# Kernel tuning notes

Hardware: AMD Instinct MI355X
Metric: run time of the kernel (lower is better)

The kernel has to match this reference:

```python
import jax, jax.numpy as jnp
import numpy as np

RADIUS = 12
SIGMA = 5.0
T0 = 0.1
TOP_PERCENT = 0.1
CURVE_STEPS = 8


def _gaussian_kernel():
    xs = jnp.arange(-RADIUS, RADIUS + 1, dtype=jnp.float32)
    k = jnp.exp(-0.5 * jnp.square(xs / SIGMA))
    k = k / jnp.sum(k)
    k2 = k[:, None] * k[None, :]
    # depthwise kernel (O=3, I/group=1, 25, 25)
    return jnp.tile(k2[None, None], (3, 1, 1, 1))


def tanh01(x):
    return (jnp.tanh(x) + 1) / 2


def tanh_range(l, r):
    return lambda x: tanh01(x) * (r - l) + l


def _parse_params(p):
    omega = tanh_range(0.1, 1.0)(p[:, 0:1])                          # (B,1)
    wb_mask = jnp.array([0.0, 1.0, 1.0], dtype=p.dtype)[None]
    wb = jnp.exp(tanh_range(-0.5, 0.5)(p[:, 1:4] * wb_mask))         # (B,3)
    lg = jnp.log(jnp.asarray(3.0, dtype=p.dtype))
    gamma = jnp.exp(tanh_range(-lg, lg)(p[:, 4:5]))                  # (B,1)
    tone = tanh_range(0.5, 2.0)(p[:, 5:13].reshape(-1, 1, 8)[:, None, None, :])  # (B,1,1,1,8)
    contrast = jnp.tanh(p[:, 13:14])                                 # (B,1)
    sharpen = tanh_range(0.0, 5.0)(p[:, 14:15])                      # (B,1)
    return omega, wb, gamma, tone, contrast, sharpen


def _apply_defog(x, omega):
    # mirror `if x.min() < 0: x = (x+1)/2` in a jit-safe way
    x = jnp.where(jnp.min(x) < 0, (x + 1) / 2, x)
    B, C, H, W = x.shape
    dark = jnp.min(x, axis=1)                                        # (B,H,W)
    k = int(H * W * TOP_PERCENT)
    flat = dark.reshape(B, H * W)
    _, idx = jax.lax.top_k(flat, k)                                  # (B,k)
    xf = x.reshape(B, C, H * W)
    sel = jnp.take_along_axis(xf, idx[:, None, :], axis=2)           # (B,C,k)
    A = jnp.max(sel, axis=2)[:, :, None, None]                       # (B,C,1,1)
    t = jnp.clip(1 - omega[:, :, None] * dark, T0, 1.0)[:, None]     # (B,1,H,W)
    J = (x - A) / t + A
    return jnp.clip(J, 0.0, 1.0)


def _apply_white_balance(image, wb):
    denom = (0.27 * wb[:, 0] + 0.67 * wb[:, 1] + 0.06 * wb[:, 2] + 1e-05)[:, None]
    p = wb / denom
    return image * p[:, :, None, None]


def _apply_gamma(image, gamma):
    g = jnp.tile(gamma, (1, 3))[:, :, None, None]                    # (B,3,1,1)
    return jnp.power(jnp.maximum(image, 1e-4), g)


def _apply_tone(image, tone):
    tone_sum = jnp.sum(tone, axis=-1) + 1e-30                        # (B,1,1,1)
    total = jnp.zeros_like(image)
    for i in range(CURVE_STEPS):
        total = total + jnp.clip(image - 1.0 * i / CURVE_STEPS, 0.0, 1.0 / CURVE_STEPS) * tone[:, :, :, :, i]
    return total * CURVE_STEPS / tone_sum


def _apply_contrast(image, contrast):
    # faithful to source: rgb2lum indexes the LAST axis (W), giving (B,3,H,1)
    lum = (0.27 * image[:, :, :, 0] + 0.67 * image[:, :, :, 1] + 0.06 * image[:, :, :, 2])[:, :, :, None]
    lum = jnp.clip(lum, 0.0, 1.0)
    contrast_lum = -jnp.cos(jnp.pi * lum) * 0.5 + 0.5
    contrast_image = image / (lum + 1e-6) * contrast_lum
    c = contrast[:, :, None, None]                                   # (B,1,1,1)
    return (1 - c) * image + c * contrast_image


def _apply_sharpen(image, sharpen):
    kernel = _gaussian_kernel()
    blurred = jax.lax.conv_general_dilated(
        image, kernel, window_strides=(1, 1),
        padding=[(RADIUS, RADIUS), (RADIUS, RADIUS)],
        dimension_numbers=('NCHW', 'OIHW', 'NCHW'),
        feature_group_count=3)
    s = sharpen[:, None, None, :]                                    # (B,1,1,1)
    return (image - blurred) * s + image


def setup_inputs() -> dict:
    key = jax.random.key(0)
    k1, k2 = jax.random.split(key)
    x = jax.random.uniform(k1, (16, 3, 512, 512), dtype=jnp.float32)
    params = jax.random.normal(k2, (16, 15), dtype=jnp.float32)
    return {"x": x, "params": params}


def reference(x, params):
    omega, wb, gamma, tone, contrast, sharpen = _parse_params(params)
    image = _apply_defog(x, omega)
    image = _apply_white_balance(image, wb)
    image = _apply_gamma(image, gamma)
    image = _apply_tone(image, tone)
    image = _apply_contrast(image, contrast)
    image = _apply_sharpen(image, sharpen)
    return jax.nn.sigmoid(image)
```

## Files before the change

kernel.cpp:

```cpp
#include <hip/hip_runtime.h>
#include <math.h>

#define NB 16
#define NC 3
#define NH 512
#define NW 512
#define NHW (NH*NW)
#define KSEL 26214u
#define PI_F 3.14159265358979f
#define LOG2E_F 1.44269504f
#define POISON_U32 0xAAAAAAAAu

typedef _Float16 half4v __attribute__((ext_vector_type(4)));
typedef _Float16 half8v __attribute__((ext_vector_type(8)));
typedef float    float4v __attribute__((ext_vector_type(4)));

#define TMPH_OFF   0
#define PCH_OFF    (NB*NC*NHW/2)
#define HIST_OFF   (PCH_OFF + NB*NC*NHW/2)
#define BMAX_OFF   (HIST_OFF + NB*256)
#define AVAL_OFF   (BMAX_OFF + NB*768)
#define PBUF_OFF   (AVAL_OFF + NB*3)
#define GW_OFF     (PBUF_OFF + NB*32)

__device__ __forceinline__ float fast_rcp(float x)  { return __builtin_amdgcn_rcpf(x); }
__device__ __forceinline__ float fast_exp2(float x) { return __builtin_amdgcn_exp2f(x); }
__device__ __forceinline__ float fast_log2(float x) { return __builtin_amdgcn_logf(x); }

__device__ __forceinline__ int swzf4(int f) {
  int t = f & 7;
  int g = ((f >> 3) & 1) ? ((3 - t) & 7) : t;
  return (f & ~7) | g;
}

__device__ __forceinline__ float chain_tt(float xv, float dv, float omega, float Aval,
                                          float wbp, float g, const float* tone) {
  float t = fminf(fmaxf(1.f - omega*dv, 0.1f), 1.f);
  float J = (xv - Aval)*fast_rcp(t) + Aval;
  J = fminf(fmaxf(J, 0.f), 1.f);
  float v = J * wbp;
  float u = fast_exp2(g * fast_log2(fmaxf(v, 1e-4f)));
  float tt = 0.f;
#pragma unroll
  for (int i = 0; i < 8; i++)
    tt = fmaf(fminf(fmaxf(u - 0.125f*(float)i, 0.f), 0.125f), tone[i], tt);
  return tt;
}

__device__ __forceinline__ float4 chain4(float4 v, float4 d, float omega, float A,
                                         float wbp, float g, const float* tone) {
  float4 r;
  r.x = chain_tt(v.x, d.x, omega, A, wbp, g, tone);
  r.y = chain_tt(v.y, d.y, omega, A, wbp, g, tone);
  r.z = chain_tt(v.z, d.z, omega, A, wbp, g, tone);
  r.w = chain_tt(v.w, d.w, omega, A, wbp, g, tone);
  return r;
}

__global__ __launch_bounds__(256) void k_stats(const float* __restrict__ x,
                                               unsigned* __restrict__ hist,
                                               unsigned* __restrict__ binmax) {
  __shared__ unsigned lh[8*256];
  __shared__ unsigned lbm[8][768];
  int tid = threadIdx.x, b = blockIdx.y;
  for (int i = tid; i < 8*256; i += 256) lh[i] = 0u;
  for (int i = tid; i < 8*768; i += 256) ((unsigned*)lbm)[i] = 0u;
  __syncthreads();
  const float4* x0 = (const float4*)(x + (size_t)b*NC*NHW);
  const float4* x1 = x0 + NHW/4;
  const float4* x2 = x1 + NHW/4;
  unsigned* lhm = lh + (tid & 7)*256;
  unsigned* bmr = lbm[tid & 7];
  int base = blockIdx.x*1024 + tid;
#pragma unroll
  for (int it = 0; it < 4; it++) {
    int i = base + it*256;
    float4 a = x0[i], g = x1[i], r = x2[i];
    float dv[4] = { fminf(fminf(a.x,g.x),r.x), fminf(fminf(a.y,g.y),r.y),
                    fminf(fminf(a.z,g.z),r.z), fminf(fminf(a.w,g.w),r.w) };
    float av[4] = {a.x,a.y,a.z,a.w}, gv[4] = {g.x,g.y,g.z,g.w}, rv[4] = {r.x,r.y,r.z,r.w};
#pragma unroll
    for (int q = 0; q < 4; q++) {
      unsigned bin = __float_as_uint(dv[q]) >> 24;
      atomicAdd(&lhm[bin], 1u);
      atomicMax(&bmr[bin],       __float_as_uint(av[q]));
      atomicMax(&bmr[256 + bin], __float_as_uint(gv[q]));
      atomicMax(&bmr[512 + bin], __float_as_uint(rv[q]));
    }
  }
  __syncthreads();
  {
    unsigned s = 0;
    for (int r2 = 0; r2 < 8; r2++) s += lh[r2*256 + tid];
    if (s) atomicAdd(&hist[b*256 + tid], s);
  }
  for (int idx = tid; idx < 768; idx += 256) {
    unsigned m = lbm[0][idx];
#pragma unroll
    for (int r2 = 1; r2 < 8; r2++) m = max(m, lbm[r2][idx]);
    if (m) atomicMin(&binmax[b*768 + idx], 0x7FFFFFFFu - m);
  }
}

__global__ void k_scan(const unsigned* __restrict__ hist,
                       const unsigned* __restrict__ binmax,
                       float* __restrict__ avals,
                       const float* __restrict__ p, float* __restrict__ pbuf,
                       float* __restrict__ gw) {
  int b = blockIdx.x, tid = threadIdx.x;
  if (tid < 64) {
    int lane = tid;
    unsigned cnt[4], s = 0;
#pragma unroll
    for (int j = 0; j < 4; j++) {
      cnt[j] = hist[b*256 + (255 - (lane*4+j))] - POISON_U32;
      s += cnt[j];
    }
    unsigned inc = s;
    for (int off = 1; off < 64; off <<= 1) {
      unsigned n = __shfl_up(inc, off);
      if (lane >= off) inc += n;
    }
    unsigned excl = inc - s;
    bool found = (excl < KSEL && KSEL <= inc);
    int localBin = 0;
    if (found) {
      unsigned run = excl; int binj = 0;
#pragma unroll
      for (int j = 0; j < 4; j++) {
        unsigned nb = run + cnt[j];
        if (KSEL > run && KSEL <= nb) binj = j;
        run = nb;
      }
      localBin = 255 - (lane*4 + binj);
    }
    unsigned long long mask = __ballot(found ? 1 : 0);
    int src = (int)__ffsll((long long)mask) - 1;
    int bstar = __shfl(localBin, src);
#pragma unroll
    for (int c = 0; c < 3; c++) {
      float m = 0.f;
#pragma unroll
      for (int j = 0; j < 4; j++) {
        int bin = 255 - (lane*4 + j);
        if (bin >= bstar) {
          unsigned enc = binmax[b*768 + c*256 + bin];
          unsigned bits = (enc <= 0x7FFFFFFFu) ? (0x7FFFFFFFu - enc) : 0u;
          m = fmaxf(m, __uint_as_float(bits));
        }
      }
      for (int off = 1; off < 64; off <<= 1) m = fmaxf(m, __shfl_xor(m, off));
      if (lane == 0) avals[b*3 + c] = m;
    }
  } else if (tid == 64) {
    const float* pp = p + b*15;
    float* ob = pbuf + b*32;
    float omega = (tanhf(pp[0])+1.f)*0.5f*0.9f + 0.1f;
    float wb0 = 1.0f;
    float wb1 = expf((tanhf(pp[2])+1.f)*0.5f - 0.5f);
    float wb2 = expf((tanhf(pp[3])+1.f)*0.5f - 0.5f);
    float denom = 0.27f*wb0 + 0.67f*wb1 + 0.06f*wb2 + 1e-5f;
    float lg = logf(3.0f);
    float g = expf((tanhf(pp[4])+1.f)*0.5f*(2.f*lg) - lg);
    float ts = 0.f, tone[8];
    for (int i = 0; i < 8; i++) { tone[i] = (tanhf(pp[5+i])+1.f)*0.5f*1.5f + 0.5f; ts += tone[i]; }
    ts += 1e-30f;
    ob[0] = omega; ob[1] = wb0/denom; ob[2] = wb1/denom; ob[3] = wb2/denom; ob[4] = g;
    for (int i = 0; i < 8; i++) ob[5+i] = tone[i];
    ob[13] = 8.0f/ts;
    ob[14] = tanhf(pp[13]);
    ob[15] = (tanhf(pp[14])+1.f)*0.5f*5.0f;
  } else if (tid == 65 && b == 0) {
    float wv[25], wsum = 0.f;
    for (int i = 0; i < 25; i++) { float d = (float)(i-12)/5.0f; wv[i] = expf(-0.5f*d*d); wsum += wv[i]; }
    for (int i = 0; i < 25; i++) gw[i] = wv[i]/wsum;
  }
}

__global__ __launch_bounds__(256) void k_hblur(
    const float* __restrict__ x, const float* __restrict__ pbuf,
    const float* __restrict__ avals, const float* __restrict__ gw,
    _Float16* __restrict__ tmph, _Float16* __restrict__ pch) {
  __shared__ __align__(16) float pcp[4][544];
  int tid = threadIdx.x;
  int row = tid >> 6, lane = tid & 63;
  int b = blockIdx.y, c = blockIdx.z;
  int h = blockIdx.x*4 + row;
  const float* pb = pbuf + b*32;
  float omega = pb[0], g = pb[4], ts = pb[13], cc = pb[14];
  float wbp = pb[1 + c];
  float tone[8];
#pragma unroll
  for (int i = 0; i < 8; i++) tone[i] = pb[5+i];
  float A = avals[b*3 + c];
  if (lane < 4) {
    float4 z; z.x = 0.f; z.y = 0.f; z.z = 0.f; z.w = 0.f;
    *(float4*)(&pcp[row][0] + swzf4(lane)*4) = z;
    *(float4*)(&pcp[row][0] + swzf4(132 + lane)*4) = z;
  }
  const float* xbase = x + (size_t)b*3*NHW + (size_t)h*NW;
  const float4* xr0 = (const float4*)(xbase);
  const float4* xr1 = (const float4*)(xbase + NHW);
  const float4* xr2 = (const float4*)(xbase + 2*(size_t)NHW);
  float4 pk;
#pragma unroll
  for (int m = 0; m < 2; m++) {
    int i4 = lane + m*64;
    float4 v0 = xr0[i4], v1 = xr1[i4], v2 = xr2[i4];
    float4 d;
    d.x = fminf(fminf(v0.x,v1.x),v2.x); d.y = fminf(fminf(v0.y,v1.y),v2.y);
    d.z = fminf(fminf(v0.z,v1.z),v2.z); d.w = fminf(fminf(v0.w,v1.w),v2.w);
    float4 vc = (c == 0) ? v0 : (c == 1) ? v1 : v2;
    float4 p = chain4(vc, d, omega, A, wbp, g, tone);
    *(float4*)(&pcp[row][0] + swzf4(4 + i4)*4) = p;
    if (m == 0) pk = p;
  }
  __syncthreads();
  float rf;
  {
    float t0 = 0.f;
    if (lane == 0) {
      float l = fminf(fmaxf((0.27f*pk.x + 0.67f*pk.y + 0.06f*pk.z)*ts, 0.f), 1.f);
      t0 = ts*((1.f - cc) + cc*(0.5f - 0.5f*__cosf(PI_F*l))*fast_rcp(l + 1e-6f));
    }
    rf = __shfl(t0, 0);
  }
  float kw[25];
#pragma unroll
  for (int j = 0; j < 25; j++) kw[j] = gw[j];
  float4 w[8];
#pragma unroll
  for (int r = 0; r < 8; r++) w[r] = *(const float4*)(&pcp[row][0] + swzf4(2*lane + 1 + r)*4);
  float acc[8] = {0,0,0,0,0,0,0,0};
#pragma unroll
  for (int r = 0; r < 8; r++) {
    float vs[4] = {w[r].x, w[r].y, w[r].z, w[r].w};
#pragma unroll
    for (int q = 0; q < 4; q++) {
      int idx = r*4 + q;
#pragma unroll
      for (int i = 0; i < 8; i++) {
        int j = idx - i;
        if (j >= 0 && j < 25) acc[i] = fmaf(kw[j], vs[q], acc[i]);
      }
    }
  }
  size_t off = ((size_t)b*3 + c)*NHW + (size_t)h*NW + lane*8;
  half8v th;
#pragma unroll
  for (int i = 0; i < 8; i++) th[i] = (_Float16)(acc[i]*rf);
  *(half8v*)(tmph + off) = th;
  half8v ph;
  ph[0] = (_Float16)(w[3].x*rf); ph[1] = (_Float16)(w[3].y*rf);
  ph[2] = (_Float16)(w[3].z*rf); ph[3] = (_Float16)(w[3].w*rf);
  ph[4] = (_Float16)(w[4].x*rf); ph[5] = (_Float16)(w[4].y*rf);
  ph[6] = (_Float16)(w[4].z*rf); ph[7] = (_Float16)(w[4].w*rf);
  *(half8v*)(pch + off) = ph;
}

#define VSTR 68
__global__ __launch_bounds__(256) void k_vblur(
    const _Float16* __restrict__ tmph, const _Float16* __restrict__ pch,
    const float* __restrict__ pbuf, const float* __restrict__ gw,
    float* __restrict__ out) {
  __shared__ _Float16 sh[152*VSTR];
  int tid = threadIdx.x;
  int bc = blockIdx.z, b = bc/3;
  int w0 = blockIdx.x*64, h0 = blockIdx.y*128;
  const _Float16* tr = tmph + (size_t)bc*NHW;
  for (int idx = tid; idx < 152*8; idx += 256) {
    int r = idx >> 3, seg = idx & 7;
    int gh = h0 - 12 + r;
    uint4 v = make_uint4(0u,0u,0u,0u);
    if (gh >= 0 && gh < NH) v = *(const uint4*)(tr + (size_t)gh*NW + w0 + seg*8);
    _Float16* dst = &sh[r*VSTR + seg*8];
    uint2 lo; lo.x = v.x; lo.y = v.y;
    uint2 hi; hi.x = v.z; hi.y = v.w;
    *(uint2*)dst = lo;
    *(uint2*)(dst + 4) = hi;
  }
  __syncthreads();
  float kw[25];
#pragma unroll
  for (int j = 0; j < 25; j++) kw[j] = gw[j];
  int wq = tid & 15, rg = tid >> 4;
  int rowbase = rg*8;
  float4v acc[8];
#pragma unroll
  for (int i = 0; i < 8; i++) acc[i] = (float4v)0.f;
#pragma unroll
  for (int r = 0; r < 32; r++) {
    half4v hv = *(const half4v*)&sh[(rowbase + r)*VSTR + wq*4];
    float4v v = __builtin_convertvector(hv, float4v);
#pragma unroll
    for (int i = 0; i < 8; i++) {
      int j = r - i;
      if (j >= 0 && j < 25) acc[i] += kw[j]*v;
    }
  }
  float sharp = pbuf[b*32 + 15];
#pragma unroll
  for (int i = 0; i < 8; i++) {
    int h = h0 + rowbase + i;
    size_t off = (size_t)bc*NHW + (size_t)h*NW + w0 + wq*4;
    half4v pcv = *(const half4v*)(pch + off);
    float4v pc = __builtin_convertvector(pcv, float4v);
    float4v res = (pc - acc[i])*sharp + pc;
    float4v o;
    o.x = fast_rcp(1.f + fast_exp2(-res.x*LOG2E_F));
    o.y = fast_rcp(1.f + fast_exp2(-res.y*LOG2E_F));
    o.z = fast_rcp(1.f + fast_exp2(-res.z*LOG2E_F));
    o.w = fast_rcp(1.f + fast_exp2(-res.w*LOG2E_F));
    *(float4v*)(out + off) = o;
  }
}

extern "C" void kernel_launch(void* const* d_in, const int* in_sizes, int n_in,
                              void* d_out, int out_size, void* d_ws, size_t ws_size,
                              hipStream_t stream) {
  const float* x = (const float*)d_in[0];
  const float* params = (const float*)d_in[1];
  float* out = (float*)d_out;
  float* ws = (float*)d_ws;

  _Float16* tmph = (_Float16*)(ws + TMPH_OFF);
  _Float16* pch  = (_Float16*)(ws + PCH_OFF);
  unsigned* hist   = (unsigned*)(ws + HIST_OFF);
  unsigned* binmax = (unsigned*)(ws + BMAX_OFF);
  float* avals = ws + AVAL_OFF;
  float* pbuf  = ws + PBUF_OFF;
  float* gw    = ws + GW_OFF;

  k_stats<<<dim3(64, NB), 256, 0, stream>>>(x, hist, binmax);
  k_scan<<<NB, 128, 0, stream>>>(hist, binmax, avals, params, pbuf, gw);
  k_hblur<<<dim3(NH/4, NB, 3), 256, 0, stream>>>(x, pbuf, avals, gw, tmph, pch);
  k_vblur<<<dim3(NW/64, NH/128, NB*NC), 256, 0, stream>>>(tmph, pch, pbuf, gw, out);
}
```

Baseline: 152.9 us.

## Process all three channels per hblur block and use wave shuffles for halo

The horizontal blur kernel now handles all three channels of a row in one block. It computes the dark-channel min once, so x is read once instead of three times across separate channel blocks. The shared-memory row buffer and __syncthreads are replaced with cross-lane shuffles that fetch neighbour pixels for the 25-tap horizontal convolution. The trade-off is more shuffle instructions and more registers per thread, and only a third as many blocks are launched.

```diff
diff --git a/kernel.cpp b/kernel.cpp
--- a/kernel.cpp
+++ b/kernel.cpp
@@ -27,12 +27,6 @@
 __device__ __forceinline__ float fast_exp2(float x) { return __builtin_amdgcn_exp2f(x); }
 __device__ __forceinline__ float fast_log2(float x) { return __builtin_amdgcn_logf(x); }
 
-__device__ __forceinline__ int swzf4(int f) {
-  int t = f & 7;
-  int g = ((f >> 3) & 1) ? ((3 - t) & 7) : t;
-  return (f & ~7) | g;
-}
-
 __device__ __forceinline__ float chain_tt(float xv, float dv, float omega, float Aval,
                                           float wbp, float g, const float* tone) {
   float t = fminf(fmaxf(1.f - omega*dv, 0.1f), 1.f);
@@ -45,16 +39,6 @@
   for (int i = 0; i < 8; i++)
     tt = fmaf(fminf(fmaxf(u - 0.125f*(float)i, 0.f), 0.125f), tone[i], tt);
   return tt;
-}
-
-__device__ __forceinline__ float4 chain4(float4 v, float4 d, float omega, float A,
-                                         float wbp, float g, const float* tone) {
-  float4 r;
-  r.x = chain_tt(v.x, d.x, omega, A, wbp, g, tone);
-  r.y = chain_tt(v.y, d.y, omega, A, wbp, g, tone);
-  r.z = chain_tt(v.z, d.z, omega, A, wbp, g, tone);
-  r.w = chain_tt(v.w, d.w, omega, A, wbp, g, tone);
-  return r;
 }
 
 __global__ __launch_bounds__(256) void k_stats(const float* __restrict__ x,
@@ -181,81 +165,111 @@
     const float* __restrict__ x, const float* __restrict__ pbuf,
     const float* __restrict__ avals, const float* __restrict__ gw,
     _Float16* __restrict__ tmph, _Float16* __restrict__ pch) {
-  __shared__ __align__(16) float pcp[4][544];
   int tid = threadIdx.x;
-  int row = tid >> 6, lane = tid & 63;
-  int b = blockIdx.y, c = blockIdx.z;
-  int h = blockIdx.x*4 + row;
+  int wv = tid >> 6, lane = tid & 63;
+  int b = blockIdx.y;
+  int h = blockIdx.x*4 + wv;
   const float* pb = pbuf + b*32;
   float omega = pb[0], g = pb[4], ts = pb[13], cc = pb[14];
-  float wbp = pb[1 + c];
+  float wbp[3] = {pb[1], pb[2], pb[3]};
   float tone[8];
 #pragma unroll
   for (int i = 0; i < 8; i++) tone[i] = pb[5+i];
-  float A = avals[b*3 + c];
-  if (lane < 4) {
-    float4 z; z.x = 0.f; z.y = 0.f; z.z = 0.f; z.w = 0.f;
-    *(float4*)(&pcp[row][0] + swzf4(lane)*4) = z;
-    *(float4*)(&pcp[row][0] + swzf4(132 + lane)*4) = z;
-  }
+  float Av[3] = {avals[b*3], avals[b*3+1], avals[b*3+2]};
+  float kw[25];
+#pragma unroll
+  for (int j = 0; j < 25; j++) kw[j] = gw[j];
+
   const float* xbase = x + (size_t)b*3*NHW + (size_t)h*NW;
-  const float4* xr0 = (const float4*)(xbase);
-  const float4* xr1 = (const float4*)(xbase + NHW);
-  const float4* xr2 = (const float4*)(xbase + 2*(size_t)NHW);
-  float4 pk;
-#pragma unroll
-  for (int m = 0; m < 2; m++) {
-    int i4 = lane + m*64;
-    float4 v0 = xr0[i4], v1 = xr1[i4], v2 = xr2[i4];
-    float4 d;
-    d.x = fminf(fminf(v0.x,v1.x),v2.x); d.y = fminf(fminf(v0.y,v1.y),v2.y);
-    d.z = fminf(fminf(v0.z,v1.z),v2.z); d.w = fminf(fminf(v0.w,v1.w),v2.w);
-    float4 vc = (c == 0) ? v0 : (c == 1) ? v1 : v2;
-    float4 p = chain4(vc, d, omega, A, wbp, g, tone);
-    *(float4*)(&pcp[row][0] + swzf4(4 + i4)*4) = p;
-    if (m == 0) pk = p;
-  }
-  __syncthreads();
-  float rf;
+  float cv[8], d[8];
   {
-    float t0 = 0.f;
-    if (lane == 0) {
-      float l = fminf(fmaxf((0.27f*pk.x + 0.67f*pk.y + 0.06f*pk.z)*ts, 0.f), 1.f);
-      t0 = ts*((1.f - cc) + cc*(0.5f - 0.5f*__cosf(PI_F*l))*fast_rcp(l + 1e-6f));
-    }
-    rf = __shfl(t0, 0);
-  }
-  float kw[25];
-#pragma unroll
-  for (int j = 0; j < 25; j++) kw[j] = gw[j];
-  float4 w[8];
-#pragma unroll
-  for (int r = 0; r < 8; r++) w[r] = *(const float4*)(&pcp[row][0] + swzf4(2*lane + 1 + r)*4);
-  float acc[8] = {0,0,0,0,0,0,0,0};
-#pragma unroll
-  for (int r = 0; r < 8; r++) {
-    float vs[4] = {w[r].x, w[r].y, w[r].z, w[r].w};
+    const float4* r0 = (const float4*)xbase;
+    const float4* r1 = (const float4*)(xbase + NHW);
+    const float4* r2 = (const float4*)(xbase + 2*(size_t)NHW);
+    float4 a0 = r0[2*lane], a1 = r0[2*lane+1];
+    float4 b0 = r1[2*lane], b1 = r1[2*lane+1];
+    float4 c0 = r2[2*lane], c1 = r2[2*lane+1];
+    d[0] = fminf(fminf(a0.x,b0.x),c0.x); d[1] = fminf(fminf(a0.y,b0.y),c0.y);
+    d[2] = fminf(fminf(a0.z,b0.z),c0.z); d[3] = fminf(fminf(a0.w,b0.w),c0.w);
+    d[4] = fminf(fminf(a1.x,b1.x),c1.x); d[5] = fminf(fminf(a1.y,b1.y),c1.y);
+    d[6] = fminf(fminf(a1.z,b1.z),c1.z); d[7] = fminf(fminf(a1.w,b1.w),c1.w);
+    cv[0]=a0.x; cv[1]=a0.y; cv[2]=a0.z; cv[3]=a0.w;
+    cv[4]=a1.x; cv[5]=a1.y; cv[6]=a1.z; cv[7]=a1.w;
+  }
+  bool okm1 = (lane >= 1), okm2 = (lane >= 2);
+  bool okp1 = (lane <= 62), okp2 = (lane <= 61);
+
+#pragma unroll
+  for (int c = 0; c < 3; c++) {
+    if (c > 0) {
+      const float4* xr = (const float4*)(xbase + (size_t)c*NHW);
+      asm volatile("" : "+v"(xr));
+      float4 u0 = xr[2*lane], u1 = xr[2*lane+1];
+      cv[0]=u0.x; cv[1]=u0.y; cv[2]=u0.z; cv[3]=u0.w;
+      cv[4]=u1.x; cv[5]=u1.y; cv[6]=u1.z; cv[7]=u1.w;
+    }
+    float pv[8];
+#pragma unroll
+    for (int k = 0; k < 8; k++) pv[k] = chain_tt(cv[k], d[k], omega, Av[c], wbp[c], g, tone);
+    float l0 = __shfl(pv[0], 0), l1 = __shfl(pv[1], 0), l2 = __shfl(pv[2], 0);
+    float l = fminf(fmaxf((0.27f*l0 + 0.67f*l1 + 0.06f*l2)*ts, 0.f), 1.f);
+    float rf = ts*((1.f - cc) + cc*(0.5f - 0.5f*__cosf(PI_F*l))*fast_rcp(l + 1e-6f));
+    float acc[8] = {0,0,0,0,0,0,0,0};
+#pragma unroll
+    for (int q = 0; q < 8; q++)
+#pragma unroll
+      for (int j = 0; j < 8; j++)
+        acc[j] = fmaf(kw[q-j+12], pv[q], acc[j]);
+#pragma unroll
+    for (int q = 0; q < 8; q++) {
+      float v = __shfl(pv[q], lane-1);
+      v = okm1 ? v : 0.f;
+#pragma unroll
+      for (int j = 0; j < 8; j++) {
+        int t = -8 + q - j;
+        if (t >= -12) acc[j] = fmaf(kw[t+12], v, acc[j]);
+      }
+    }
+#pragma unroll
+    for (int q = 0; q < 8; q++) {
+      float v = __shfl(pv[q], lane+1);
+      v = okp1 ? v : 0.f;
+#pragma unroll
+      for (int j = 0; j < 8; j++) {
+        int t = 8 + q - j;
+        if (t <= 12) acc[j] = fmaf(kw[t+12], v, acc[j]);
+      }
+    }
+#pragma unroll
+    for (int q = 4; q < 8; q++) {
+      float v = __shfl(pv[q], lane-2);
+      v = okm2 ? v : 0.f;
+#pragma unroll
+      for (int j = 0; j < 8; j++) {
+        int t = -16 + q - j;
+        if (t >= -12) acc[j] = fmaf(kw[t+12], v, acc[j]);
+      }
+    }
 #pragma unroll
     for (int q = 0; q < 4; q++) {
-      int idx = r*4 + q;
-#pragma unroll
-      for (int i = 0; i < 8; i++) {
-        int j = idx - i;
-        if (j >= 0 && j < 25) acc[i] = fmaf(kw[j], vs[q], acc[i]);
-      }
-    }
-  }
-  size_t off = ((size_t)b*3 + c)*NHW + (size_t)h*NW + lane*8;
-  half8v th;
-#pragma unroll
-  for (int i = 0; i < 8; i++) th[i] = (_Float16)(acc[i]*rf);
-  *(half8v*)(tmph + off) = th;
-  half8v ph;
-  ph[0] = (_Float16)(w[3].x*rf); ph[1] = (_Float16)(w[3].y*rf);
-  ph[2] = (_Float16)(w[3].z*rf); ph[3] = (_Float16)(w[3].w*rf);
-  ph[4] = (_Float16)(w[4].x*rf); ph[5] = (_Float16)(w[4].y*rf);
-  ph[6] = (_Float16)(w[4].z*rf); ph[7] = (_Float16)(w[4].w*rf);
-  *(half8v*)(pch + off) = ph;
+      float v = __shfl(pv[q], lane+2);
+      v = okp2 ? v : 0.f;
+#pragma unroll
+      for (int j = 0; j < 8; j++) {
+        int t = 16 + q - j;
+        if (t <= 12) acc[j] = fmaf(kw[t+12], v, acc[j]);
+      }
+    }
+    size_t off = ((size_t)b*3 + c)*NHW + (size_t)h*NW + lane*8;
+    half8v th, ph;
+#pragma unroll
+    for (int k = 0; k < 8; k++) {
+      th[k] = (_Float16)(acc[k]*rf);
+      ph[k] = (_Float16)(pv[k]*rf);
+    }
+    *(half8v*)(tmph + off) = th;
+    *(half8v*)(pch + off) = ph;
+  }
 }
 
 #define VSTR 68
@@ -333,6 +347,6 @@
 
   k_stats<<<dim3(64, NB), 256, 0, stream>>>(x, hist, binmax);
   k_scan<<<NB, 128, 0, stream>>>(hist, binmax, avals, params, pbuf, gw);
-  k_hblur<<<dim3(NH/4, NB, 3), 256, 0, stream>>>(x, pbuf, avals, gw, tmph, pch);
+  k_hblur<<<dim3(NH/4, NB), 256, 0, stream>>>(x, pbuf, avals, gw, tmph, pch);
   k_vblur<<<dim3(NW/64, NH/128, NB*NC), 256, 0, stream>>>(tmph, pch, pbuf, gw, out);
 }
```

Result: faster. 146.3 us (-4.3%).
